# Performance work log

Hardware: AMD Instinct MI355X
Metric: run time of the kernel (lower is better)

## Reference

```python
import jax, jax.numpy as jnp
import numpy as np

B, T, C, H = 4, 2048, 1024, 16
D = C // H  # head_dim = 64


def setup_inputs() -> dict:
    key = jax.random.key(0)
    ks = jax.random.split(key, 10)
    s = 1.0 / np.sqrt(C)
    inp = {
        "x": jax.random.normal(ks[0], (B, T, C), dtype=jnp.float32),
        "attention_mask": jnp.ones((B, T), dtype=jnp.int32),
        "Wq": jax.random.normal(ks[1], (C, C), dtype=jnp.float32) * s,
        "bq": jnp.zeros((C,), dtype=jnp.float32),
        "Wk": jax.random.normal(ks[2], (C, C), dtype=jnp.float32) * s,
        "bk": jnp.zeros((C,), dtype=jnp.float32),
        "Wv": jax.random.normal(ks[3], (C, C), dtype=jnp.float32) * s,
        "bv": jnp.zeros((C,), dtype=jnp.float32),
        "Wp": jax.random.normal(ks[4], (C, C), dtype=jnp.float32) * s,
        "bp": jnp.zeros((C,), dtype=jnp.float32),
    }
    return inp


def reference(x, attention_mask, Wq, bq, Wk, bk, Wv, bv, Wp, bp):
    # x: [B,T,C] -> q,k,v: [B,H,T,D]
    def heads(y):
        return y.reshape(B, T, H, D).transpose(0, 2, 1, 3)

    q = heads(x @ Wq + bq)
    k = heads(x @ Wk + bk)
    v = heads(x @ Wv + bv)

    scale = 1.0 / np.sqrt(D)
    att = jnp.einsum("bhqd,bhkd->bhqk", q, k) * scale  # [B,H,T,T]

    causal = jnp.tril(jnp.ones((T, T), dtype=bool))  # [T,T]
    mask = causal[None, None, :, :] & (attention_mask[:, None, None, :] != 0)
    att = jnp.where(mask, att, -jnp.inf)
    att = jax.nn.softmax(att, axis=-1)
    # dropout is identity in eval mode

    y = jnp.einsum("bhqk,bhkd->bhqd", att, v)  # [B,H,T,D]
    y = y.transpose(0, 2, 1, 3).reshape(B, T, C)
    return y @ Wp + bp
```

## Files before the change

### kernel.cpp

```cpp
#include <hip/hip_runtime.h>

#define BB 4
#define TT 2048
#define CC 1024
#define HH 16
#define DD 64

typedef unsigned short u16;
typedef unsigned int u32;
typedef __bf16 bf16;
typedef __attribute__((ext_vector_type(8))) bf16 bf16x8;
typedef __attribute__((ext_vector_type(8))) u16 u16x8;
typedef __attribute__((ext_vector_type(4))) u16 u16x4;
typedef __attribute__((ext_vector_type(4))) float f32x4;

static __device__ __forceinline__ u16 f2b(float f) {
  unsigned u = __builtin_bit_cast(unsigned, f);
  u += 0x7fffu + ((u >> 16) & 1u);
  return (u16)(u >> 16);
}
static __device__ __forceinline__ u16 bfc(float f) {
  return __builtin_bit_cast(u16, (__bf16)f);
}
static __device__ __forceinline__ float max3f(float a, float b, float c) {
  float d;
  asm("v_max3_f32 %0, %1, %2, %3" : "=v"(d) : "v"(a), "v"(b), "v"(c));
  return d;
}

__global__ __launch_bounds__(256) void prep_kernel(
    const float* __restrict__ x, const int* __restrict__ am,
    const float* __restrict__ w0, const float* __restrict__ w1,
    const float* __restrict__ w2, const float* __restrict__ w3,
    u16* __restrict__ xb, u16* __restrict__ wqkvT, u16* __restrict__ wpT,
    float* __restrict__ gm, u32* __restrict__ fwords) {
  __shared__ float t[32][33];
  const int bid = blockIdx.x, tid = threadIdx.x;
  if (bid < 4096) {
    int i = bid * 256 + tid;
    const float4* p4 = reinterpret_cast<const float4*>(x) + (size_t)i * 2;
    float4 a = p4[0], b = p4[1];
    u16x8 o;
    o[0] = f2b(a.x); o[1] = f2b(a.y); o[2] = f2b(a.z); o[3] = f2b(a.w);
    o[4] = f2b(b.x); o[5] = f2b(b.y); o[6] = f2b(b.z); o[7] = f2b(b.w);
    *reinterpret_cast<u16x8*>(xb + (size_t)i * 8) = o;
  } else if (bid < 8192) {
    int r2 = bid - 4096;
    int z = r2 >> 10, rem = r2 & 1023;
    int k0 = (rem & 31) * 32, n0 = (rem >> 5) * 32;
    const float* src = z == 0 ? w0 : z == 1 ? w1 : z == 2 ? w2 : w3;
    u16* dst = z < 3 ? wqkvT + (size_t)z * CC * CC : wpT;
    int tx = tid & 31, ty = tid >> 5;
#pragma unroll
    for (int i = 0; i < 4; ++i)
      t[ty + i * 8][tx] = src[(size_t)(k0 + ty + i * 8) * CC + n0 + tx];
    __syncthreads();
#pragma unroll
    for (int i = 0; i < 4; ++i)
      dst[(size_t)(n0 + ty + i * 8) * CC + k0 + tx] = f2b(t[tx][ty + i * 8]);
  } else {
    __shared__ u32 sf[32];
    int b = bid - 8192;
    int lane = tid & 63, w = tid >> 6;
#pragma unroll
    for (int j = 0; j < 8; ++j) {
      int c = w * 8 + j;
      int i = c * 64 + lane;
      int v = am[b * TT + i];
      gm[b * TT + i] = v ? 0.f : -1e30f;
      unsigned long long bal = __ballot(v != 0);
      if (lane == 0) sf[c] = (bal == ~0ull) ? 1u : 0u;
    }
    __syncthreads();
    if (tid == 0) {
      u32 fw = 0;
      for (int c = 0; c < 32; ++c) fw |= sf[c] << c;
      fwords[b] = fw;
    }
  }
}

__global__ __launch_bounds__(256) void qkv_gemm_kernel(
    const u16* __restrict__ A, const u16* __restrict__ Bt,
    const float* __restrict__ bq, const float* __restrict__ bk, const float* __restrict__ bv,
    u16* __restrict__ q_out, u16* __restrict__ k_out, u16* __restrict__ v_out) {
  __shared__ __align__(16) char LDS[65536];
  const int tid = threadIdx.x, lane = tid & 63, w = tid >> 6;
  const int wm = w >> 1, wn = w & 1;
  const int lq = lane & 15, g = lane >> 4;
  const int m0 = blockIdx.x * 128, n0 = blockIdx.y * 128;
  const int l3 = lane >> 3;
  const int swb = ((lane & 7) ^ (l3 & 7)) * 16;
  f32x4 acc[4][4] = {};

  auto STAGE = [&](int db, int kt) {
    const int ko = kt * 128;
#pragma unroll
    for (int r = 0; r < 4; ++r) {
      int rb = r * 32 + w * 8;
      __builtin_amdgcn_global_load_lds(
          (const __attribute__((address_space(1))) void*)(
              (const char*)A + (size_t)(m0 + rb + l3) * 2048 + ko + swb),
          (__attribute__((address_space(3))) void*)(LDS + db * 16384 + rb * 128), 16, 0, 0);
      __builtin_amdgcn_global_load_lds(
          (const __attribute__((address_space(1))) void*)(
              (const char*)Bt + (size_t)(n0 + rb + l3) * 2048 + ko + swb),
          (__attribute__((address_space(3))) void*)(LDS + 32768 + db * 16384 + rb * 128), 16, 0, 0);
    }
  };

  const int acol0 = (g * 16) ^ ((lq & 7) << 4);
  const int acol1 = (64 + g * 16) ^ ((lq & 7) << 4);
  const int aBase = wm * 8192 + lq * 128;
  const int bBase = 32768 + wn * 8192 + lq * 128;

  STAGE(0, 0);
  STAGE(1, 1);
  for (int kt = 0; kt < 16; ++kt) {
    if (kt == 15) asm volatile("s_waitcnt vmcnt(0)" ::: "memory");
    else          asm volatile("s_waitcnt vmcnt(8)" ::: "memory");
    asm volatile("s_barrier" ::: "memory");
    const int db = kt & 1;
    const char* la = LDS + db * 16384 + aBase;
    const char* lb = LDS + db * 16384 + bBase;
    bf16x8 af[4][2], bfr[4][2];
#pragma unroll
    for (int i = 0; i < 4; ++i) {
      af[i][0] = *reinterpret_cast<const bf16x8*>(la + i * 2048 + acol0);
      af[i][1] = *reinterpret_cast<const bf16x8*>(la + i * 2048 + acol1);
      bfr[i][0] = *reinterpret_cast<const bf16x8*>(lb + i * 2048 + acol0);
      bfr[i][1] = *reinterpret_cast<const bf16x8*>(lb + i * 2048 + acol1);
    }
    asm volatile("s_waitcnt lgkmcnt(0)" ::: "memory");
    __builtin_amdgcn_sched_barrier(0);
    __builtin_amdgcn_s_setprio(1);
#pragma unroll
    for (int i = 0; i < 4; ++i)
#pragma unroll
      for (int j = 0; j < 4; ++j) {
        acc[i][j] = __builtin_amdgcn_mfma_f32_16x16x32_bf16(af[i][0], bfr[j][0], acc[i][j], 0, 0, 0);
        acc[i][j] = __builtin_amdgcn_mfma_f32_16x16x32_bf16(af[i][1], bfr[j][1], acc[i][j], 0, 0, 0);
      }
    __builtin_amdgcn_s_setprio(0);
    asm volatile("s_barrier" ::: "memory");
    if (kt + 2 < 16) STAGE(db, kt + 2);
  }

  const int g3 = n0 >> 10;
  const int mrow = m0 + wm * 64;
  const int ncol = n0 + wn * 64;
  if (g3 < 2) {
    u16* dst = g3 == 0 ? q_out : k_out;
    const float* bias = g3 == 0 ? bq : bk;
    const float scl = g3 == 0 ? 0.18033688f : 1.0f;
#pragma unroll
    for (int i = 0; i < 4; ++i)
#pragma unroll
      for (int j = 0; j < 4; ++j) {
        int n = ncol + j * 16 + lq;
        int h = (n >> 6) & 15, d = n & 63;
        float bb = bias[n & 1023];
#pragma unroll
        for (int r = 0; r < 4; ++r) {
          int m = mrow + i * 16 + g * 4 + r;
          int b = m >> 11, t = m & 2047;
          dst[(((size_t)(b * HH + h)) * TT + t) * DD + d] = f2b((acc[i][j][r] + bb) * scl);
        }
      }
  } else {
#pragma unroll
    for (int i = 0; i < 4; ++i)
#pragma unroll
      for (int j = 0; j < 4; ++j) {
        int n = ncol + j * 16 + lq;
        int h = (n >> 6) & 15, d = n & 63;
        float bb = bv[n & 1023];
        int mb = mrow + i * 16 + g * 4;
        int b = mb >> 11, t = mb & 2047;
        u16x4 vv;
#pragma unroll
        for (int r = 0; r < 4; ++r) vv[r] = f2b(acc[i][j][r] + bb);
        *reinterpret_cast<u16x4*>(v_out + (((size_t)(b * HH + h)) * DD + d) * TT + t) = vv;
      }
  }
}

__global__ __launch_bounds__(256) void proj_gemm_kernel(
    const u16* __restrict__ A, const u16* __restrict__ Bt,
    const float* __restrict__ bias, float* __restrict__ f_out) {
  __shared__ __align__(16) char LDS[65536];
  const int tid = threadIdx.x, lane = tid & 63, w = tid >> 6;
  const int wm = w >> 1, wn = w & 1;
  const int lq = lane & 15, g = lane >> 4;
  const int m0 = blockIdx.x * 128, n0 = blockIdx.y * 128;
  const int l3 = lane >> 3;
  const int swb = ((lane & 7) ^ (l3 & 7)) * 16;
  f32x4 acc[4][4] = {};

  auto STAGE = [&](int db, int kt) {
    const int ko = kt * 128;
#pragma unroll
    for (int r = 0; r < 4; ++r) {
      int rb = r * 32 + w * 8;
      __builtin_amdgcn_global_load_lds(
          (const __attribute__((address_space(1))) void*)(
              (const char*)A + (size_t)(m0 + rb + l3) * 2048 + ko + swb),
          (__attribute__((address_space(3))) void*)(LDS + db * 16384 + rb * 128), 16, 0, 0);
      __builtin_amdgcn_global_load_lds(
          (const __attribute__((address_space(1))) void*)(
              (const char*)Bt + (size_t)(n0 + rb + l3) * 2048 + ko + swb),
          (__attribute__((address_space(3))) void*)(LDS + 32768 + db * 16384 + rb * 128), 16, 0, 0);
    }
  };

  const int acol0 = (g * 16) ^ ((lq & 7) << 4);
  const int acol1 = (64 + g * 16) ^ ((lq & 7) << 4);
  const int aBase = wm * 8192 + lq * 128;
  const int bBase = 32768 + wn * 8192 + lq * 128;

  STAGE(0, 0);
  STAGE(1, 1);
  for (int kt = 0; kt < 16; ++kt) {
    if (kt == 15) asm volatile("s_waitcnt vmcnt(0)" ::: "memory");
    else          asm volatile("s_waitcnt vmcnt(8)" ::: "memory");
    asm volatile("s_barrier" ::: "memory");
    const int db = kt & 1;
    const char* la = LDS + db * 16384 + aBase;
    const char* lb = LDS + db * 16384 + bBase;
    bf16x8 af[4][2], bfr[4][2];
#pragma unroll
    for (int i = 0; i < 4; ++i) {
      af[i][0] = *reinterpret_cast<const bf16x8*>(la + i * 2048 + acol0);
      af[i][1] = *reinterpret_cast<const bf16x8*>(la + i * 2048 + acol1);
      bfr[i][0] = *reinterpret_cast<const bf16x8*>(lb + i * 2048 + acol0);
      bfr[i][1] = *reinterpret_cast<const bf16x8*>(lb + i * 2048 + acol1);
    }
    asm volatile("s_waitcnt lgkmcnt(0)" ::: "memory");
    __builtin_amdgcn_sched_barrier(0);
    __builtin_amdgcn_s_setprio(1);
#pragma unroll
    for (int i = 0; i < 4; ++i)
#pragma unroll
      for (int j = 0; j < 4; ++j) {
        acc[i][j] = __builtin_amdgcn_mfma_f32_16x16x32_bf16(af[i][0], bfr[j][0], acc[i][j], 0, 0, 0);
        acc[i][j] = __builtin_amdgcn_mfma_f32_16x16x32_bf16(af[i][1], bfr[j][1], acc[i][j], 0, 0, 0);
      }
    __builtin_amdgcn_s_setprio(0);
    asm volatile("s_barrier" ::: "memory");
    if (kt + 2 < 16) STAGE(db, kt + 2);
  }

  const int mrow = m0 + wm * 64;
  const int ncol = n0 + wn * 64;
#pragma unroll
  for (int i = 0; i < 4; ++i)
#pragma unroll
    for (int j = 0; j < 4; ++j)
#pragma unroll
      for (int r = 0; r < 4; ++r) {
        int m = mrow + i * 16 + g * 4 + r;
        int n = ncol + j * 16 + lq;
        f_out[(size_t)m * CC + n] = acc[i][j][r] + bias[n];
      }
}

__global__ __launch_bounds__(256, 2) void attn_kernel(
    const u16* __restrict__ Q, const u16* __restrict__ K, const u16* __restrict__ Vt,
    const float* __restrict__ gm, const u32* __restrict__ fwords, u16* __restrict__ Y) {
  __shared__ __align__(16) char LDS[51200];
  const int flat = blockIdx.x;
  const int xcd = flat & 7, idx = flat >> 3;
  const int bh = xcd * 8 + (idx & 7);
  const int jb = 15 - (idx >> 3);
  const int b = bh >> 4, h = bh & 15;
  const int tid = threadIdx.x, lane = tid & 63, w = tid >> 6;
  const int lq = lane & 15, g = lane >> 4;
  const int qt = 4 * jb + w;
  const int q0 = qt * 32;
  const int nkt = (qt >> 1) + 1;
  const int nktm = 2 * jb + 2;
  const u32 fw = fwords[b];

  const u16* Qb = Q + (size_t)bh * TT * DD;
  const char* Kb = (const char*)(K + (size_t)bh * TT * DD);
  const char* Vb = (const char*)(Vt + (size_t)bh * DD * TT);

  const int l3 = lane >> 3, l7 = lane & 7;
  const int swb = (l7 * 16) ^ (l3 << 4);
  const char* kp0 = Kb + (2 * w + 0) * 1024 + l3 * 128 + swb;
  const char* kp1 = Kb + (2 * w + 1) * 1024 + l3 * 128 + swb;
  const char* vp0 = Vb + (size_t)((2 * w + 0) * 8 + l3) * 4096 + swb;
  const char* vp1 = Vb + (size_t)((2 * w + 1) * 8 + l3) * 4096 + swb;

  const int sw2 = (lq & 7) << 4;
  const int fb0 = lq * 128 + ((g * 16) ^ sw2);
  const int fb1 = lq * 128 + (((64) + g * 16) ^ sw2);
  const int pwb = 32768 + w * 4608 + lq * 144 + g * 8;
  const int prb = 32768 + w * 4608 + lq * 144 + g * 16;

  auto STAGE = [&](int buf, int kt2) {
    const int ko = kt2 * 8192, vo = kt2 * 128, lb = buf * 8192;
    __builtin_amdgcn_global_load_lds(
        (const __attribute__((address_space(1))) void*)(kp0 + ko),
        (__attribute__((address_space(3))) void*)(LDS + lb + (2 * w + 0) * 1024), 16, 0, 0);
    __builtin_amdgcn_global_load_lds(
        (const __attribute__((address_space(1))) void*)(kp1 + ko),
        (__attribute__((address_space(3))) void*)(LDS + lb + (2 * w + 1) * 1024), 16, 0, 0);
    __builtin_amdgcn_global_load_lds(
        (const __attribute__((address_space(1))) void*)(vp0 + vo),
        (__attribute__((address_space(3))) void*)(LDS + 16384 + lb + (2 * w + 0) * 1024), 16, 0, 0);
    __builtin_amdgcn_global_load_lds(
        (const __attribute__((address_space(1))) void*)(vp1 + vo),
        (__attribute__((address_space(3))) void*)(LDS + 16384 + lb + (2 * w + 1) * 1024), 16, 0, 0);
  };

  bf16x8 qf[2][2];
#pragma unroll
  for (int n = 0; n < 2; ++n)
#pragma unroll
    for (int ks = 0; ks < 2; ++ks)
      qf[n][ks] = *reinterpret_cast<const bf16x8*>(
          Qb + (size_t)(q0 + n * 16 + lq) * DD + ks * 32 + g * 8);

  const u16x8 onesu = {0x3F80, 0x3F80, 0x3F80, 0x3F80, 0x3F80, 0x3F80, 0x3F80, 0x3F80};
  const bf16x8 ones = __builtin_bit_cast(bf16x8, onesu);

  f32x4 o[4][2] = {};
  f32x4 l_acc[2] = {};
  float mrun[2] = {-1e30f, -1e30f};
  const f32x4 z4 = {0.f, 0.f, 0.f, 0.f};

  STAGE(0, 0);
  STAGE(1, 1);

  auto TILE = [&](int BUF, int kt) {
    if (kt < nktm - 1)
      asm volatile("s_waitcnt vmcnt(4)" ::: "memory");
    else
      asm volatile("s_waitcnt vmcnt(0)" ::: "memory");
    asm volatile("s_barrier" ::: "memory");

    if (kt < nkt) {
      const int kv0 = kt * 64;
      bf16x8 kf0[4], kf1[4];
#pragma unroll
      for (int m = 0; m < 4; ++m) {
        kf0[m] = *reinterpret_cast<const bf16x8*>(LDS + BUF * 8192 + m * 2048 + fb0);
        kf1[m] = *reinterpret_cast<const bf16x8*>(LDS + BUF * 8192 + m * 2048 + fb1);
      }
      f32x4 s[4][2];
      __builtin_amdgcn_s_setprio(1);
#pragma unroll
      for (int m = 0; m < 4; ++m)
#pragma unroll
        for (int n = 0; n < 2; ++n) {
          s[m][n] = __builtin_amdgcn_mfma_f32_16x16x32_bf16(kf0[m], qf[n][0], z4, 0, 0, 0);
          s[m][n] = __builtin_amdgcn_mfma_f32_16x16x32_bf16(kf1[m], qf[n][1], s[m][n], 0, 0, 0);
        }
      __builtin_amdgcn_s_setprio(0);

      if (!((fw >> kt) & 1u)) {
#pragma unroll
        for (int m = 0; m < 4; ++m) {
          float4 mv = *reinterpret_cast<const float4*>(gm + b * TT + kv0 + m * 16 + g * 4);
#pragma unroll
          for (int n = 0; n < 2; ++n) {
            s[m][n][0] += mv.x; s[m][n][1] += mv.y;
            s[m][n][2] += mv.z; s[m][n][3] += mv.w;
          }
        }
      }
      if (kt == nkt - 1) {
#pragma unroll
        for (int n = 0; n < 2; ++n) {
          const int q = q0 + n * 16 + lq;
#pragma unroll
          for (int m = 0; m < 4; ++m)
#pragma unroll
            for (int r = 0; r < 4; ++r) {
              int kv = kv0 + m * 16 + g * 4 + r;
              s[m][n][r] = (kv <= q) ? s[m][n][r] : -1e30f;
            }
        }
      }

#pragma unroll
      for (int n = 0; n < 2; ++n) {
        float m1 = max3f(s[0][n][0], s[0][n][1], s[0][n][2]);
        float m2 = max3f(s[0][n][3], s[1][n][0], s[1][n][1]);
        float m3 = max3f(s[1][n][2], s[1][n][3], s[2][n][0]);
        float m4 = max3f(s[2][n][1], s[2][n][2], s[2][n][3]);
        float m5 = max3f(s[3][n][0], s[3][n][1], s[3][n][2]);
        float rm = fmaxf(max3f(m1, m2, m3), max3f(m4, m5, s[3][n][3]));
        if (!__all(rm <= mrun[n] + 8.f)) {
          float rg = fmaxf(rm, __shfl_xor(rm, 16));
          rg = fmaxf(rg, __shfl_xor(rg, 32));
          float mnew = fmaxf(mrun[n], rg);
          float corr = __builtin_exp2f(mrun[n] - mnew);
          mrun[n] = mnew;
          l_acc[n] *= corr;
#pragma unroll
          for (int nd = 0; nd < 4; ++nd)
#pragma unroll
            for (int r = 0; r < 4; ++r) o[nd][n][r] *= corr;
        }
        const float mn = mrun[n];
#pragma unroll
        for (int m = 0; m < 4; ++m) {
          float p0 = __builtin_exp2f(s[m][n][0] - mn);
          float p1 = __builtin_exp2f(s[m][n][1] - mn);
          float p2 = __builtin_exp2f(s[m][n][2] - mn);
          float p3 = __builtin_exp2f(s[m][n][3] - mn);
          u32 wa, wb;
          asm("v_cvt_pk_bf16_f32 %0, %1, %2" : "=v"(wa) : "v"(p0), "v"(p1));
          asm("v_cvt_pk_bf16_f32 %0, %1, %2" : "=v"(wb) : "v"(p2), "v"(p3));
          uint2 pw; pw.x = wa; pw.y = wb;
          *reinterpret_cast<uint2*>(LDS + pwb + n * 2304 + m * 32) = pw;
        }
      }

      asm volatile("s_waitcnt lgkmcnt(0)" ::: "memory");
      __builtin_amdgcn_sched_barrier(0);

      __builtin_amdgcn_s_setprio(1);
#pragma unroll
      for (int ks = 0; ks < 2; ++ks) {
        const int fb = ks ? fb1 : fb0;
        bf16x8 pf0 = *reinterpret_cast<const bf16x8*>(LDS + prb + 0 * 2304 + ks * 64);
        bf16x8 pf1 = *reinterpret_cast<const bf16x8*>(LDS + prb + 1 * 2304 + ks * 64);
#pragma unroll
        for (int nd = 0; nd < 4; ++nd) {
          bf16x8 vf = *reinterpret_cast<const bf16x8*>(LDS + 16384 + BUF * 8192 + nd * 2048 + fb);
          o[nd][0] = __builtin_amdgcn_mfma_f32_16x16x32_bf16(vf, pf0, o[nd][0], 0, 0, 0);
          o[nd][1] = __builtin_amdgcn_mfma_f32_16x16x32_bf16(vf, pf1, o[nd][1], 0, 0, 0);
        }
        l_acc[0] = __builtin_amdgcn_mfma_f32_16x16x32_bf16(ones, pf0, l_acc[0], 0, 0, 0);
        l_acc[1] = __builtin_amdgcn_mfma_f32_16x16x32_bf16(ones, pf1, l_acc[1], 0, 0, 0);
      }
      __builtin_amdgcn_s_setprio(0);
    }

    asm volatile("s_barrier" ::: "memory");
    if (kt + 2 < nktm) STAGE(BUF, kt + 2);
  };

  for (int kt = 0; kt < nktm; kt += 2) {
    TILE(0, kt);
    TILE(1, kt + 1);
  }

#pragma unroll
  for (int n = 0; n < 2; ++n) {
    float inv = 1.0f / l_acc[n][0];
    const int q = q0 + n * 16 + lq;
#pragma unroll
    for (int nd = 0; nd < 4; ++nd) {
      u16x4 yv;
#pragma unroll
      for (int r = 0; r < 4; ++r) yv[r] = bfc(o[nd][n][r] * inv);
      *reinterpret_cast<u16x4*>(
          Y + ((size_t)(b * TT + q)) * CC + h * DD + nd * 16 + g * 4) = yv;
    }
  }
}

extern "C" void kernel_launch(void* const* d_in, const int* in_sizes, int n_in,
                              void* d_out, int out_size, void* d_ws, size_t ws_size,
                              hipStream_t stream) {
  const float* x  = (const float*)d_in[0];
  const int*   am = (const int*)d_in[1];
  const float* Wq = (const float*)d_in[2];
  const float* bq = (const float*)d_in[3];
  const float* Wk = (const float*)d_in[4];
  const float* bk = (const float*)d_in[5];
  const float* Wv = (const float*)d_in[6];
  const float* bv = (const float*)d_in[7];
  const float* Wp = (const float*)d_in[8];
  const float* bp = (const float*)d_in[9];
  float* out = (float*)d_out;

  char* ws = (char*)d_ws;
  u16* xb    = (u16*)(ws);
  u16* wqkvT = (u16*)(ws + (16ull << 20));
  u16* wpT   = (u16*)(ws + (22ull << 20));
  u16* qw    = (u16*)(ws + (24ull << 20));
  u16* kw    = (u16*)(ws + (40ull << 20));
  u16* vw    = (u16*)(ws + (56ull << 20));
  u16* yb    = (u16*)(ws + (72ull << 20));
  float* gm  = (float*)d_out;
  u32* fwords = (u32*)((char*)d_out + (64ull << 10));

  prep_kernel<<<dim3(8196), 256, 0, stream>>>(
      x, am, Wq, Wk, Wv, Wp, xb, wqkvT, wpT, gm, fwords);
  qkv_gemm_kernel<<<dim3(64, 24), 256, 0, stream>>>(
      xb, wqkvT, bq, bk, bv, qw, kw, vw);
  attn_kernel<<<dim3(1024), 256, 0, stream>>>(qw, kw, vw, gm, fwords, yb);
  proj_gemm_kernel<<<dim3(64, 8), 256, 0, stream>>>(yb, wpT, bp, out);
}
```

Before: 157.4 us.

## Triple-buffer attention K/V tiles and swizzle GEMM block order for XCD locality

The attention kernel goes from double to triple buffering of K/V tiles in LDS, so the prefetch for tile kt+2 is issued right after the top barrier and the second barrier per iteration is removed. LDS grows to about 66 KB per block, which may limit occupancy at two blocks per CU. Separately, both GEMM kernels remap block indices so consecutive blocks on the same XCD share weight or activation tiles, aiming for better L2 reuse.

```diff
diff --git a/kernel.cpp b/kernel.cpp
--- a/kernel.cpp
+++ b/kernel.cpp
@@ -88,7 +88,9 @@
   const int tid = threadIdx.x, lane = tid & 63, w = tid >> 6;
   const int wm = w >> 1, wn = w & 1;
   const int lq = lane & 15, g = lane >> 4;
-  const int m0 = blockIdx.x * 128, n0 = blockIdx.y * 128;
+  const int flat = blockIdx.y * 64 + blockIdx.x;
+  const int swz = (flat & 7) * 192 + (flat >> 3);
+  const int m0 = (swz & 63) * 128, n0 = (swz >> 6) * 128;
   const int l3 = lane >> 3;
   const int swb = ((lane & 7) ^ (l3 & 7)) * 16;
   f32x4 acc[4][4] = {};
@@ -192,7 +194,9 @@
   const int tid = threadIdx.x, lane = tid & 63, w = tid >> 6;
   const int wm = w >> 1, wn = w & 1;
   const int lq = lane & 15, g = lane >> 4;
-  const int m0 = blockIdx.x * 128, n0 = blockIdx.y * 128;
+  const int flat = blockIdx.y * 64 + blockIdx.x;
+  const int swz = (flat & 7) * 64 + (flat >> 3);
+  const int m0 = (swz & 63) * 128, n0 = (swz >> 6) * 128;
   const int l3 = lane >> 3;
   const int swb = ((lane & 7) ^ (l3 & 7)) * 16;
   f32x4 acc[4][4] = {};
@@ -267,7 +271,7 @@
 __global__ __launch_bounds__(256, 2) void attn_kernel(
     const u16* __restrict__ Q, const u16* __restrict__ K, const u16* __restrict__ Vt,
     const float* __restrict__ gm, const u32* __restrict__ fwords, u16* __restrict__ Y) {
-  __shared__ __align__(16) char LDS[51200];
+  __shared__ __align__(16) char LDS[67584];
   const int flat = blockIdx.x;
   const int xcd = flat & 7, idx = flat >> 3;
   const int bh = xcd * 8 + (idx & 7);
@@ -295,8 +299,8 @@
   const int sw2 = (lq & 7) << 4;
   const int fb0 = lq * 128 + ((g * 16) ^ sw2);
   const int fb1 = lq * 128 + (((64) + g * 16) ^ sw2);
-  const int pwb = 32768 + w * 4608 + lq * 144 + g * 8;
-  const int prb = 32768 + w * 4608 + lq * 144 + g * 16;
+  const int pwb = 49152 + w * 4608 + lq * 144 + g * 8;
+  const int prb = 49152 + w * 4608 + lq * 144 + g * 16;
 
   auto STAGE = [&](int buf, int kt2) {
     const int ko = kt2 * 8192, vo = kt2 * 128, lb = buf * 8192;
@@ -308,10 +312,10 @@
         (__attribute__((address_space(3))) void*)(LDS + lb + (2 * w + 1) * 1024), 16, 0, 0);
     __builtin_amdgcn_global_load_lds(
         (const __attribute__((address_space(1))) void*)(vp0 + vo),
-        (__attribute__((address_space(3))) void*)(LDS + 16384 + lb + (2 * w + 0) * 1024), 16, 0, 0);
+        (__attribute__((address_space(3))) void*)(LDS + 24576 + lb + (2 * w + 0) * 1024), 16, 0, 0);
     __builtin_amdgcn_global_load_lds(
         (const __attribute__((address_space(1))) void*)(vp1 + vo),
-        (__attribute__((address_space(3))) void*)(LDS + 16384 + lb + (2 * w + 1) * 1024), 16, 0, 0);
+        (__attribute__((address_space(3))) void*)(LDS + 24576 + lb + (2 * w + 1) * 1024), 16, 0, 0);
   };
 
   bf16x8 qf[2][2];
@@ -333,20 +337,28 @@
   STAGE(0, 0);
   STAGE(1, 1);
 
-  auto TILE = [&](int BUF, int kt) {
+  int bcur = 0;
+  for (int kt = 0; kt < nktm; ++kt) {
     if (kt < nktm - 1)
       asm volatile("s_waitcnt vmcnt(4)" ::: "memory");
     else
       asm volatile("s_waitcnt vmcnt(0)" ::: "memory");
     asm volatile("s_barrier" ::: "memory");
 
+    if (kt + 2 < nktm) {
+      int b2 = bcur - 1; if (b2 < 0) b2 = 2;
+      STAGE(b2, kt + 2);
+    }
+
     if (kt < nkt) {
       const int kv0 = kt * 64;
+      const char* kbuf = LDS + bcur * 8192;
+      const char* vbuf = LDS + 24576 + bcur * 8192;
       bf16x8 kf0[4], kf1[4];
 #pragma unroll
       for (int m = 0; m < 4; ++m) {
-        kf0[m] = *reinterpret_cast<const bf16x8*>(LDS + BUF * 8192 + m * 2048 + fb0);
-        kf1[m] = *reinterpret_cast<const bf16x8*>(LDS + BUF * 8192 + m * 2048 + fb1);
+        kf0[m] = *reinterpret_cast<const bf16x8*>(kbuf + m * 2048 + fb0);
+        kf1[m] = *reinterpret_cast<const bf16x8*>(kbuf + m * 2048 + fb1);
       }
       f32x4 s[4][2];
       __builtin_amdgcn_s_setprio(1);
@@ -430,7 +442,7 @@
         bf16x8 pf1 = *reinterpret_cast<const bf16x8*>(LDS + prb + 1 * 2304 + ks * 64);
 #pragma unroll
         for (int nd = 0; nd < 4; ++nd) {
-          bf16x8 vf = *reinterpret_cast<const bf16x8*>(LDS + 16384 + BUF * 8192 + nd * 2048 + fb);
+          bf16x8 vf = *reinterpret_cast<const bf16x8*>(vbuf + nd * 2048 + fb);
           o[nd][0] = __builtin_amdgcn_mfma_f32_16x16x32_bf16(vf, pf0, o[nd][0], 0, 0, 0);
           o[nd][1] = __builtin_amdgcn_mfma_f32_16x16x32_bf16(vf, pf1, o[nd][1], 0, 0, 0);
         }
@@ -440,13 +452,7 @@
       __builtin_amdgcn_s_setprio(0);
     }
 
-    asm volatile("s_barrier" ::: "memory");
-    if (kt + 2 < nktm) STAGE(BUF, kt + 2);
-  };
-
-  for (int kt = 0; kt < nktm; kt += 2) {
-    TILE(0, kt);
-    TILE(1, kt + 1);
+    bcur = (bcur == 2) ? 0 : bcur + 1;
   }
 
 #pragma unroll
```

New measurement: 183.7 us. +16.7%, slower.
